# Kernel tuning notes

Measured on AMD Instinct MI355X. Metric: run time of the kernel, lower is better.

Reference implementation:

```python
import jax, jax.numpy as jnp
import numpy as np

D_MODEL = 64
SEQ_LEN = 9
MAX_SL = 50
TIMESTAMP = 56
ACTION_NUM = 300
BATCH = 65536


def setup_inputs() -> dict:
    key = jax.random.key(0)
    ks = jax.random.split(key, 8)
    input_actions = jax.random.randint(ks[0], (BATCH, SEQ_LEN), 0, ACTION_NUM + 1)
    emb_table = jax.random.normal(ks[1], (ACTION_NUM + 1, D_MODEL), jnp.float32) * 0.02
    emb_table = emb_table.at[0].set(0.0)  # padding_idx=0
    M_w = jax.random.normal(ks[2], (MAX_SL, D_MODEL, D_MODEL), jnp.float32) * 0.05
    M_b = jax.random.normal(ks[3], (MAX_SL, D_MODEL), jnp.float32) * 0.05
    W_w = jax.random.normal(ks[4], (TIMESTAMP, D_MODEL, D_MODEL), jnp.float32) * 0.05
    W_b = jax.random.normal(ks[5], (TIMESTAMP, D_MODEL), jnp.float32) * 0.05
    out_w = jax.random.normal(ks[6], (ACTION_NUM, D_MODEL), jnp.float32) * 0.05
    out_b = jax.random.normal(ks[7], (ACTION_NUM,), jnp.float32) * 0.05
    return {"input_actions": input_actions, "emb_table": emb_table,
            "M_w": M_w, "M_b": M_b, "W_w": W_w, "W_b": W_b,
            "out_w": out_w, "out_b": out_b}


def reference(input_actions, emb_table, M_w, M_b, W_w, W_b, out_w, out_b):
    B, S = input_actions.shape
    d = emb_table.shape[1]
    ae = emb_table[input_actions]              # [B, S, d]
    ae_t = jnp.transpose(ae, (1, 0, 2))        # [S, B, d]
    # per-timestep weight selection, matching M[min(i, len(M)-1)] and W[i % timeStamp]
    m_idx = jnp.minimum(jnp.arange(S), M_w.shape[0] - 1)
    w_idx = jnp.arange(S) % W_w.shape[0]
    Mw, Mb = M_w[m_idx], M_b[m_idx]            # [S, d, d], [S, d]
    Ww, Wb = W_w[w_idx], W_b[w_idx]

    def step(hl, xs):
        x, mw, mb, ww, wb = xs
        # torch Linear: y = x @ W.T + b
        hl = jax.nn.sigmoid(x @ mw.T + mb + hl @ ww.T + wb)
        return hl, None

    hl0 = jnp.zeros((B, d), ae.dtype)
    hl, _ = jax.lax.scan(step, hl0, (ae_t, Mw, Mb, Ww, Wb))
    return hl @ out_w.T + out_b               # [B, actionNum]
```

## Files before the change

### kernel.cpp

```cpp
#include <hip/hip_runtime.h>
#include <hip/hip_bf16.h>


#define SEQ     9
#define DMODEL  64
#define ANUM    300
#define RPB     128
#define LSTR    72

#define WS_MW   0
#define WS_OW   73728
#define WS_EMB  94208
#define WS_END  113472
#define WS_BSUM_BYTES (WS_END * 2)

typedef __attribute__((ext_vector_type(8))) short  bf16x8;
typedef __attribute__((ext_vector_type(4))) float  f32x4;

__device__ __forceinline__ unsigned short f2b(float f) {
    union { float f; unsigned int u; } x; x.f = f;
    unsigned int r = x.u + 0x7FFFu + ((x.u >> 16) & 1u);
    return (unsigned short)(r >> 16);
}

__device__ __forceinline__ float sigmoid_fast(float v) {
    return __builtin_amdgcn_rcpf(1.f + __expf(-v));
}

__device__ __forceinline__ void async16(const unsigned short* g, unsigned short* l) {
    __builtin_amdgcn_global_load_lds(
        (const __attribute__((address_space(1))) unsigned int*)g,
        (__attribute__((address_space(3))) unsigned int*)l, 16, 0, 0);
}

#define PP_TOTAL (73728 + 20480 + 19264 + 576)

__global__ void prepack(const float* __restrict__ Mw, const float* __restrict__ Ww,
                        const float* __restrict__ outw, const float* __restrict__ emb,
                        const float* __restrict__ Mb, const float* __restrict__ Wb,
                        unsigned short* __restrict__ wsb, float* __restrict__ bsum)
{
    int t = blockIdx.x * 256 + threadIdx.x;
    if (t < 73728) {
        int s    = t >> 13;
        int r    = t & 8191;
        int kind = r >> 12;
        int f    = r & 4095;
        int nt   = f >> 10;
        int kb   = (f >> 9) & 1;
        int lane = (f >> 3) & 63;
        int j    = f & 7;
        int nr   = nt * 16 + (lane & 15);
        int k    = kb * 32 + ((lane >> 4) << 3) + j;
        const float* src = kind ? Ww : Mw;
        wsb[WS_MW + t] = f2b(src[(s * DMODEL + nr) * DMODEL + k]);
        return;
    }
    t -= 73728;
    if (t < 20480) {
        int j    = t & 7;
        int lane = (t >> 3) & 63;
        int kb   = (t >> 9) & 1;
        int nt   = (t >> 10) & 3;
        int cc   = t >> 12;
        int col  = cc * 64 + nt * 16 + (lane & 15);
        int k    = kb * 32 + ((lane >> 4) << 3) + j;
        float v  = (col < ANUM) ? outw[col * DMODEL + k] : 0.f;
        wsb[WS_OW + t] = f2b(v);
        return;
    }
    t -= 20480;
    if (t < 19264) { wsb[WS_EMB + t] = f2b(emb[t]); return; }
    t -= 19264;
    if (t < 576)   { bsum[t] = Mb[t] + Wb[t]; }
}

__global__ __launch_bounds__(1024, 8)
void carnn_main(const int* __restrict__ acts,
                const unsigned short* __restrict__ wsb,
                const float* __restrict__ bsum,
                const float* __restrict__ outb,
                float* __restrict__ out)
{
    __shared__ unsigned short Wf[2][8192];
    __shared__ unsigned short Hl[2][RPB * LSTR];

    const int tid  = threadIdx.x;
    const int lane = tid & 63;
    const int wv   = tid >> 6;
    const int team = wv >> 1;
    const int half = wv & 1;
    const int lrow = lane & 15;
    const int quad = lane >> 4;

    const int brow = blockIdx.x * RPB + team * 16 + lrow;
    const int hoff = (team * 16 + lrow) * LSTR + quad * 8;

    for (int i = tid; i < RPB * LSTR; i += 1024) Hl[0][i] = 0;
    async16(wsb + WS_MW + tid * 8, &Wf[0][wv * 512]);

    const unsigned short* Eb = wsb + WS_EMB;
    int idcur = acts[brow * SEQ];

    __syncthreads();

    #pragma unroll
    for (int s = 0; s < SEQ; ++s) {
        const int rb = s & 1, wb = rb ^ 1;

        const bf16x8* ex = (const bf16x8*)(Eb + idcur * DMODEL);
        bf16x8 ax0 = ex[quad];
        bf16x8 ax1 = ex[4 + quad];

        if (s + 1 < SEQ) {
            idcur = acts[brow * SEQ + s + 1];
            async16(wsb + WS_MW + (s + 1) * 8192 + tid * 8, &Wf[wb][wv * 512]);
        } else {
            if (wv < 8) async16(wsb + WS_OW + tid * 8, &Wf[wb][wv * 512]);
        }

        bf16x8 ah0 = *(const bf16x8*)&Hl[rb][hoff];
        bf16x8 ah1 = *(const bf16x8*)&Hl[rb][hoff + 32];

        #pragma unroll
        for (int ntl = 0; ntl < 2; ++ntl) {
            const int nt = half * 2 + ntl;
            const unsigned short* Mf  = &Wf[rb][nt * 1024 + lane * 8];
            const unsigned short* Wfp = &Wf[rb][4096 + nt * 1024 + lane * 8];
            bf16x8 bm0 = *(const bf16x8*)Mf;
            bf16x8 bm1 = *(const bf16x8*)(Mf + 512);
            bf16x8 bw0 = *(const bf16x8*)Wfp;
            bf16x8 bw1 = *(const bf16x8*)(Wfp + 512);

            f32x4 acc = {0.f, 0.f, 0.f, 0.f};
            acc = __builtin_amdgcn_mfma_f32_16x16x32_bf16(ax0, bm0, acc, 0, 0, 0);
            acc = __builtin_amdgcn_mfma_f32_16x16x32_bf16(ax1, bm1, acc, 0, 0, 0);
            acc = __builtin_amdgcn_mfma_f32_16x16x32_bf16(ah0, bw0, acc, 0, 0, 0);
            acc = __builtin_amdgcn_mfma_f32_16x16x32_bf16(ah1, bw1, acc, 0, 0, 0);

            const int col  = nt * 16 + lrow;
            const float bias = bsum[s * DMODEL + col];
            const int wr = (team * 16 + quad * 4) * LSTR + col;
            #pragma unroll
            for (int r = 0; r < 4; ++r) {
                float h = sigmoid_fast(acc[r] + bias);
                Hl[wb][wr + r * LSTR] = f2b(h);
            }
        }
        __syncthreads();
    }

    bf16x8 ah0 = *(const bf16x8*)&Hl[1][hoff];
    bf16x8 ah1 = *(const bf16x8*)&Hl[1][hoff + 32];
    const int rowb = blockIdx.x * RPB + team * 16 + quad * 4;

    #pragma unroll
    for (int cc = 0; cc < 5; ++cc) {
        const int rbuf = (cc + 1) & 1;
        const int wbuf = rbuf ^ 1;
        if (cc + 1 < 5 && wv < 8)
            async16(wsb + WS_OW + (cc + 1) * 4096 + tid * 8, &Wf[wbuf][wv * 512]);

        #pragma unroll
        for (int ntl = 0; ntl < 2; ++ntl) {
            const int nt = half * 2 + ntl;
            const unsigned short* Of = &Wf[rbuf][nt * 1024 + lane * 8];
            bf16x8 b0 = *(const bf16x8*)Of;
            bf16x8 b1 = *(const bf16x8*)(Of + 512);
            f32x4 acc = {0.f, 0.f, 0.f, 0.f};
            acc = __builtin_amdgcn_mfma_f32_16x16x32_bf16(ah0, b0, acc, 0, 0, 0);
            acc = __builtin_amdgcn_mfma_f32_16x16x32_bf16(ah1, b1, acc, 0, 0, 0);

            const int col = cc * 64 + nt * 16 + lrow;
            if (col < ANUM) {
                const float bias = outb[col];
                #pragma unroll
                for (int r = 0; r < 4; ++r)
                    out[(rowb + r) * ANUM + col] = acc[r] + bias;
            }
        }
        if (cc + 1 < 5) __syncthreads();
    }
}

extern "C" void kernel_launch(void* const* d_in, const int* in_sizes, int n_in,
                              void* d_out, int out_size, void* d_ws, size_t ws_size,
                              hipStream_t stream) {
    const int*   acts = (const int*)  d_in[0];
    const float* emb  = (const float*)d_in[1];
    const float* Mw   = (const float*)d_in[2];
    const float* Mb   = (const float*)d_in[3];
    const float* Ww   = (const float*)d_in[4];
    const float* Wb   = (const float*)d_in[5];
    const float* outw = (const float*)d_in[6];
    const float* outb = (const float*)d_in[7];
    float* out = (float*)d_out;
    (void)in_sizes; (void)n_in; (void)ws_size; (void)out_size;

    unsigned short* wsb = (unsigned short*)d_ws;
    float* bsum = (float*)((char*)d_ws + WS_BSUM_BYTES);

    prepack<<<(PP_TOTAL + 255) / 256, 256, 0, stream>>>(Mw, Ww, outw, emb, Mb, Wb, wsb, bsum);
    carnn_main<<<65536 / RPB, 1024, 0, stream>>>(acts, wsb, bsum, outb, out);
}
```

Before: 124.9 us.

## Halve block threads, give each wave two row tiles, read out_w from global

Cuts the block from 1024 to 512 threads. Each wave now processes two 16-row tiles and reuses the same weight fragments for both, so B-operand LDS reads are amortized. Step 0 skips the recurrent MFMAs and the Hl zero-init, since the hidden state starts at zero. The output projection reads the prepacked out_w fragments straight from global or L2 instead of double-buffering them through LDS, which removes the per-chunk barriers. In exchange, registers per thread rise and each block has fewer waves to hide latency.

New measurement: 128.1 us. 1.03x slower.

```diff
diff --git a/kernel.cpp b/kernel.cpp
--- a/kernel.cpp
+++ b/kernel.cpp
@@ -75,111 +75,135 @@
     if (t < 576)   { bsum[t] = Mb[t] + Wb[t]; }
 }
 
-__global__ __launch_bounds__(1024, 8)
+__global__ __launch_bounds__(512, 4)
 void carnn_main(const int* __restrict__ acts,
                 const unsigned short* __restrict__ wsb,
                 const float* __restrict__ bsum,
                 const float* __restrict__ outb,
                 float* __restrict__ out)
 {
-    __shared__ unsigned short Wf[2][8192];
-    __shared__ unsigned short Hl[2][RPB * LSTR];
+    __shared__ __align__(16) unsigned short Wf[2][8192];
+    __shared__ __align__(16) unsigned short Hl[2][RPB * LSTR];
 
     const int tid  = threadIdx.x;
     const int lane = tid & 63;
     const int wv   = tid >> 6;
-    const int team = wv >> 1;
+    const int rg   = wv >> 1;
     const int half = wv & 1;
     const int lrow = lane & 15;
     const int quad = lane >> 4;
 
-    const int brow = blockIdx.x * RPB + team * 16 + lrow;
-    const int hoff = (team * 16 + lrow) * LSTR + quad * 8;
-
-    for (int i = tid; i < RPB * LSTR; i += 1024) Hl[0][i] = 0;
-    async16(wsb + WS_MW + tid * 8, &Wf[0][wv * 512]);
+    const int rb0   = rg * 32 + lrow;
+    const int rb1   = rb0 + 16;
+    const int brow0 = blockIdx.x * RPB + rb0;
+    const int brow1 = brow0 + 16;
+    const int hoff0 = rb0 * LSTR + quad * 8;
+    const int hoff1 = rb1 * LSTR + quad * 8;
+
+    async16(wsb + WS_MW + tid * 8,        &Wf[0][wv * 512]);
+    async16(wsb + WS_MW + 4096 + tid * 8, &Wf[0][4096 + wv * 512]);
 
     const unsigned short* Eb = wsb + WS_EMB;
-    int idcur = acts[brow * SEQ];
+    int id0 = acts[brow0 * SEQ];
+    int id1 = acts[brow1 * SEQ];
 
     __syncthreads();
 
     #pragma unroll
     for (int s = 0; s < SEQ; ++s) {
-        const int rb = s & 1, wb = rb ^ 1;
-
-        const bf16x8* ex = (const bf16x8*)(Eb + idcur * DMODEL);
-        bf16x8 ax0 = ex[quad];
-        bf16x8 ax1 = ex[4 + quad];
+        const int rbuf = s & 1, wbuf = rbuf ^ 1;
+
+        const bf16x8* e0 = (const bf16x8*)(Eb + id0 * DMODEL);
+        const bf16x8* e1 = (const bf16x8*)(Eb + id1 * DMODEL);
+        bf16x8 ax00 = e0[quad], ax01 = e0[4 + quad];
+        bf16x8 ax10 = e1[quad], ax11 = e1[4 + quad];
 
         if (s + 1 < SEQ) {
-            idcur = acts[brow * SEQ + s + 1];
-            async16(wsb + WS_MW + (s + 1) * 8192 + tid * 8, &Wf[wb][wv * 512]);
-        } else {
-            if (wv < 8) async16(wsb + WS_OW + tid * 8, &Wf[wb][wv * 512]);
-        }
-
-        bf16x8 ah0 = *(const bf16x8*)&Hl[rb][hoff];
-        bf16x8 ah1 = *(const bf16x8*)&Hl[rb][hoff + 32];
+            id0 = acts[brow0 * SEQ + s + 1];
+            id1 = acts[brow1 * SEQ + s + 1];
+            async16(wsb + WS_MW + (s + 1) * 8192 + tid * 8,        &Wf[wbuf][wv * 512]);
+            async16(wsb + WS_MW + (s + 1) * 8192 + 4096 + tid * 8, &Wf[wbuf][4096 + wv * 512]);
+        }
+
+        bf16x8 ah00, ah01, ah10, ah11;
+        if (s > 0) {
+            ah00 = *(const bf16x8*)&Hl[rbuf][hoff0];
+            ah01 = *(const bf16x8*)&Hl[rbuf][hoff0 + 32];
+            ah10 = *(const bf16x8*)&Hl[rbuf][hoff1];
+            ah11 = *(const bf16x8*)&Hl[rbuf][hoff1 + 32];
+        }
 
         #pragma unroll
         for (int ntl = 0; ntl < 2; ++ntl) {
             const int nt = half * 2 + ntl;
-            const unsigned short* Mf  = &Wf[rb][nt * 1024 + lane * 8];
-            const unsigned short* Wfp = &Wf[rb][4096 + nt * 1024 + lane * 8];
+            const unsigned short* Mf = &Wf[rbuf][nt * 1024 + lane * 8];
             bf16x8 bm0 = *(const bf16x8*)Mf;
             bf16x8 bm1 = *(const bf16x8*)(Mf + 512);
-            bf16x8 bw0 = *(const bf16x8*)Wfp;
-            bf16x8 bw1 = *(const bf16x8*)(Wfp + 512);
-
-            f32x4 acc = {0.f, 0.f, 0.f, 0.f};
-            acc = __builtin_amdgcn_mfma_f32_16x16x32_bf16(ax0, bm0, acc, 0, 0, 0);
-            acc = __builtin_amdgcn_mfma_f32_16x16x32_bf16(ax1, bm1, acc, 0, 0, 0);
-            acc = __builtin_amdgcn_mfma_f32_16x16x32_bf16(ah0, bw0, acc, 0, 0, 0);
-            acc = __builtin_amdgcn_mfma_f32_16x16x32_bf16(ah1, bw1, acc, 0, 0, 0);
-
-            const int col  = nt * 16 + lrow;
+
+            f32x4 a0 = {0.f, 0.f, 0.f, 0.f};
+            f32x4 a1 = {0.f, 0.f, 0.f, 0.f};
+            a0 = __builtin_amdgcn_mfma_f32_16x16x32_bf16(ax00, bm0, a0, 0, 0, 0);
+            a0 = __builtin_amdgcn_mfma_f32_16x16x32_bf16(ax01, bm1, a0, 0, 0, 0);
+            a1 = __builtin_amdgcn_mfma_f32_16x16x32_bf16(ax10, bm0, a1, 0, 0, 0);
+            a1 = __builtin_amdgcn_mfma_f32_16x16x32_bf16(ax11, bm1, a1, 0, 0, 0);
+            if (s > 0) {
+                const unsigned short* Wp = &Wf[rbuf][4096 + nt * 1024 + lane * 8];
+                bf16x8 bw0 = *(const bf16x8*)Wp;
+                bf16x8 bw1 = *(const bf16x8*)(Wp + 512);
+                a0 = __builtin_amdgcn_mfma_f32_16x16x32_bf16(ah00, bw0, a0, 0, 0, 0);
+                a0 = __builtin_amdgcn_mfma_f32_16x16x32_bf16(ah01, bw1, a0, 0, 0, 0);
+                a1 = __builtin_amdgcn_mfma_f32_16x16x32_bf16(ah10, bw0, a1, 0, 0, 0);
+                a1 = __builtin_amdgcn_mfma_f32_16x16x32_bf16(ah11, bw1, a1, 0, 0, 0);
+            }
+
+            const int col   = nt * 16 + lrow;
             const float bias = bsum[s * DMODEL + col];
-            const int wr = (team * 16 + quad * 4) * LSTR + col;
+            const int wr0 = (rg * 32 + quad * 4) * LSTR + col;
+            const int wr1 = wr0 + 16 * LSTR;
             #pragma unroll
             for (int r = 0; r < 4; ++r) {
-                float h = sigmoid_fast(acc[r] + bias);
-                Hl[wb][wr + r * LSTR] = f2b(h);
+                Hl[wbuf][wr0 + r * LSTR] = f2b(sigmoid_fast(a0[r] + bias));
+                Hl[wbuf][wr1 + r * LSTR] = f2b(sigmoid_fast(a1[r] + bias));
             }
         }
         __syncthreads();
     }
 
-    bf16x8 ah0 = *(const bf16x8*)&Hl[1][hoff];
-    bf16x8 ah1 = *(const bf16x8*)&Hl[1][hoff + 32];
-    const int rowb = blockIdx.x * RPB + team * 16 + quad * 4;
+    bf16x8 ah00 = *(const bf16x8*)&Hl[1][hoff0];
+    bf16x8 ah01 = *(const bf16x8*)&Hl[1][hoff0 + 32];
+    bf16x8 ah10 = *(const bf16x8*)&Hl[1][hoff1];
+    bf16x8 ah11 = *(const bf16x8*)&Hl[1][hoff1 + 32];
+
+    const unsigned short* OWg = wsb + WS_OW;
+    const int rowb0 = blockIdx.x * RPB + rg * 32 + quad * 4;
+    const int rowb1 = rowb0 + 16;
 
     #pragma unroll
     for (int cc = 0; cc < 5; ++cc) {
-        const int rbuf = (cc + 1) & 1;
-        const int wbuf = rbuf ^ 1;
-        if (cc + 1 < 5 && wv < 8)
-            async16(wsb + WS_OW + (cc + 1) * 4096 + tid * 8, &Wf[wbuf][wv * 512]);
-
         #pragma unroll
         for (int ntl = 0; ntl < 2; ++ntl) {
             const int nt = half * 2 + ntl;
-            const unsigned short* Of = &Wf[rbuf][nt * 1024 + lane * 8];
+            const unsigned short* Of = OWg + cc * 4096 + nt * 1024 + lane * 8;
             bf16x8 b0 = *(const bf16x8*)Of;
             bf16x8 b1 = *(const bf16x8*)(Of + 512);
-            f32x4 acc = {0.f, 0.f, 0.f, 0.f};
-            acc = __builtin_amdgcn_mfma_f32_16x16x32_bf16(ah0, b0, acc, 0, 0, 0);
-            acc = __builtin_amdgcn_mfma_f32_16x16x32_bf16(ah1, b1, acc, 0, 0, 0);
+
+            f32x4 a0 = {0.f, 0.f, 0.f, 0.f};
+            f32x4 a1 = {0.f, 0.f, 0.f, 0.f};
+            a0 = __builtin_amdgcn_mfma_f32_16x16x32_bf16(ah00, b0, a0, 0, 0, 0);
+            a0 = __builtin_amdgcn_mfma_f32_16x16x32_bf16(ah01, b1, a0, 0, 0, 0);
+            a1 = __builtin_amdgcn_mfma_f32_16x16x32_bf16(ah10, b0, a1, 0, 0, 0);
+            a1 = __builtin_amdgcn_mfma_f32_16x16x32_bf16(ah11, b1, a1, 0, 0, 0);
 
             const int col = cc * 64 + nt * 16 + lrow;
             if (col < ANUM) {
                 const float bias = outb[col];
                 #pragma unroll
-                for (int r = 0; r < 4; ++r)
-                    out[(rowb + r) * ANUM + col] = acc[r] + bias;
+                for (int r = 0; r < 4; ++r) {
+                    out[(rowb0 + r) * ANUM + col] = a0[r] + bias;
+                    out[(rowb1 + r) * ANUM + col] = a1[r] + bias;
+                }
             }
         }
-        if (cc + 1 < 5) __syncthreads();
     }
 }
 
@@ -201,5 +225,5 @@
     float* bsum = (float*)((char*)d_ws + WS_BSUM_BYTES);
 
     prepack<<<(PP_TOTAL + 255) / 256, 256, 0, stream>>>(Mw, Ww, outw, emb, Mb, Wb, wsb, bsum);
-    carnn_main<<<65536 / RPB, 1024, 0, stream>>>(acts, wsb, bsum, outb, out);
-}
+    carnn_main<<<65536 / RPB, 512, 0, stream>>>(acts, wsb, bsum, outb, out);
+}
```

## Preload all step weights to LDS, per-wave rows, drop per-step block barriers

Applied to the files above, without the earlier changes.

Each block now loads most of the recurrence weights and bias sums into LDS once at the start. Each wave owns 16 batch rows and computes all 64 hidden columns itself, so the per-step __syncthreads barriers disappear and the hidden state lives in a swizzled per-wave LDS slab. The MFMA operands are transposed so weights act as A and activations as B, which gives contiguous packed output writes and vector float4 stores in the output projection. The output projection now reads out_w straight from global or L2 instead of staging it in LDS. In exchange the block uses about 158KB of LDS, which limits occupancy to one block per CU, the last step's weights are read from global memory, and the block count halves to 256.

Measured after the change: 120.4 us. 3.6% less time.

```diff
diff --git a/kernel.cpp b/kernel.cpp
--- a/kernel.cpp
+++ b/kernel.cpp
@@ -5,8 +5,6 @@
 #define SEQ     9
 #define DMODEL  64
 #define ANUM    300
-#define RPB     128
-#define LSTR    72
 
 #define WS_MW   0
 #define WS_OW   73728
@@ -14,8 +12,14 @@
 #define WS_END  113472
 #define WS_BSUM_BYTES (WS_END * 2)
 
+#define BSOFF   61440
+#define HSOFF   62592
+#define SLTOT   78976
+
 typedef __attribute__((ext_vector_type(8))) short  bf16x8;
 typedef __attribute__((ext_vector_type(4))) float  f32x4;
+
+#define MFMA __builtin_amdgcn_mfma_f32_16x16x32_bf16
 
 __device__ __forceinline__ unsigned short f2b(float f) {
     union { float f; unsigned int u; } x; x.f = f;
@@ -75,111 +79,115 @@
     if (t < 576)   { bsum[t] = Mb[t] + Wb[t]; }
 }
 
-__global__ __launch_bounds__(1024, 8)
+__global__ __launch_bounds__(1024, 4)
 void carnn_main(const int* __restrict__ acts,
                 const unsigned short* __restrict__ wsb,
                 const float* __restrict__ bsum,
                 const float* __restrict__ outb,
                 float* __restrict__ out)
 {
-    __shared__ unsigned short Wf[2][8192];
-    __shared__ unsigned short Hl[2][RPB * LSTR];
+    __shared__ __align__(16) unsigned short SL[SLTOT];
 
     const int tid  = threadIdx.x;
     const int lane = tid & 63;
     const int wv   = tid >> 6;
-    const int team = wv >> 1;
-    const int half = wv & 1;
     const int lrow = lane & 15;
     const int quad = lane >> 4;
 
-    const int brow = blockIdx.x * RPB + team * 16 + lrow;
-    const int hoff = (team * 16 + lrow) * LSTR + quad * 8;
-
-    for (int i = tid; i < RPB * LSTR; i += 1024) Hl[0][i] = 0;
-    async16(wsb + WS_MW + tid * 8, &Wf[0][wv * 512]);
+    const int brow = (blockIdx.x * 16 + wv) * 16 + lrow;
+    const int rowS = brow * SEQ;
+
+    for (int c = wv; c < 120; c += 16) {
+        const int goff = (c < 8) ? (c * 512) : ((c + 8) * 512);
+        async16(wsb + WS_MW + goff + lane * 8, &SL[c * 512]);
+    }
+    {
+        const unsigned short* bs = (const unsigned short*)bsum;
+        if (wv == 13) async16(bs + lane * 8,         &SL[BSOFF]);
+        if (wv == 14) async16(bs + 512 + lane * 8,   &SL[BSOFF + 512]);
+        if (wv == 15 && lane < 16)
+                      async16(bs + 1024 + lane * 8,  &SL[BSOFF + 1024]);
+    }
 
     const unsigned short* Eb = wsb + WS_EMB;
-    int idcur = acts[brow * SEQ];
+    int idc = acts[rowS];
+    bf16x8 xc0 = *(const bf16x8*)(Eb + idc * DMODEL + quad * 8);
+    bf16x8 xc1 = *(const bf16x8*)(Eb + idc * DMODEL + 32 + quad * 8);
+    int idn = acts[rowS + 1];
+
+    char* const SB = (char*)SL;
+    const int swz    = (lrow & 7) << 4;
+    const int hbyte  = HSOFF * 2 + wv * 2048 + lrow * 128;
+    const int rbyte0 = hbyte + ((quad * 16) ^ swz);
+    const int rbyte1 = hbyte + ((64 + quad * 16) ^ swz);
 
     __syncthreads();
+
+    const float* BSf = (const float*)&SL[BSOFF];
 
     #pragma unroll
     for (int s = 0; s < SEQ; ++s) {
-        const int rb = s & 1, wb = rb ^ 1;
-
-        const bf16x8* ex = (const bf16x8*)(Eb + idcur * DMODEL);
-        bf16x8 ax0 = ex[quad];
-        bf16x8 ax1 = ex[4 + quad];
-
+        bf16x8 xn0, xn1;
         if (s + 1 < SEQ) {
-            idcur = acts[brow * SEQ + s + 1];
-            async16(wsb + WS_MW + (s + 1) * 8192 + tid * 8, &Wf[wb][wv * 512]);
-        } else {
-            if (wv < 8) async16(wsb + WS_OW + tid * 8, &Wf[wb][wv * 512]);
+            xn0 = *(const bf16x8*)(Eb + idn * DMODEL + quad * 8);
+            xn1 = *(const bf16x8*)(Eb + idn * DMODEL + 32 + quad * 8);
+            if (s + 2 < SEQ) idn = acts[rowS + s + 2];
         }
-
-        bf16x8 ah0 = *(const bf16x8*)&Hl[rb][hoff];
-        bf16x8 ah1 = *(const bf16x8*)&Hl[rb][hoff + 32];
+        bf16x8 h0, h1;
+        if (s > 0) {
+            h0 = *(const bf16x8*)(SB + rbyte0);
+            h1 = *(const bf16x8*)(SB + rbyte1);
+        }
+        const unsigned short* WB;
+        if (s == 0)     WB = &SL[0];
+        else if (s < 8) WB = &SL[4096 + (s - 1) * 8192];
+        else            WB = wsb + WS_MW + 8 * 8192;
 
         #pragma unroll
-        for (int ntl = 0; ntl < 2; ++ntl) {
-            const int nt = half * 2 + ntl;
-            const unsigned short* Mf  = &Wf[rb][nt * 1024 + lane * 8];
-            const unsigned short* Wfp = &Wf[rb][4096 + nt * 1024 + lane * 8];
-            bf16x8 bm0 = *(const bf16x8*)Mf;
-            bf16x8 bm1 = *(const bf16x8*)(Mf + 512);
-            bf16x8 bw0 = *(const bf16x8*)Wfp;
-            bf16x8 bw1 = *(const bf16x8*)(Wfp + 512);
-
-            f32x4 acc = {0.f, 0.f, 0.f, 0.f};
-            acc = __builtin_amdgcn_mfma_f32_16x16x32_bf16(ax0, bm0, acc, 0, 0, 0);
-            acc = __builtin_amdgcn_mfma_f32_16x16x32_bf16(ax1, bm1, acc, 0, 0, 0);
-            acc = __builtin_amdgcn_mfma_f32_16x16x32_bf16(ah0, bw0, acc, 0, 0, 0);
-            acc = __builtin_amdgcn_mfma_f32_16x16x32_bf16(ah1, bw1, acc, 0, 0, 0);
-
-            const int col  = nt * 16 + lrow;
-            const float bias = bsum[s * DMODEL + col];
-            const int wr = (team * 16 + quad * 4) * LSTR + col;
-            #pragma unroll
-            for (int r = 0; r < 4; ++r) {
-                float h = sigmoid_fast(acc[r] + bias);
-                Hl[wb][wr + r * LSTR] = f2b(h);
+        for (int nt = 0; nt < 4; ++nt) {
+            const unsigned short* Mf = WB + nt * 1024 + lane * 8;
+            bf16x8 am0 = *(const bf16x8*)Mf;
+            bf16x8 am1 = *(const bf16x8*)(Mf + 512);
+            f32x4 acc = *(const f32x4*)(BSf + s * 64 + nt * 16 + quad * 4);
+            acc = MFMA(am0, xc0, acc, 0, 0, 0);
+            acc = MFMA(am1, xc1, acc, 0, 0, 0);
+            if (s > 0) {
+                const unsigned short* Wf = WB + 4096 + nt * 1024 + lane * 8;
+                bf16x8 aw0 = *(const bf16x8*)Wf;
+                bf16x8 aw1 = *(const bf16x8*)(Wf + 512);
+                acc = MFMA(aw0, h0, acc, 0, 0, 0);
+                acc = MFMA(aw1, h1, acc, 0, 0, 0);
             }
+            unsigned int u0 = (unsigned int)f2b(sigmoid_fast(acc[0]))
+                            | ((unsigned int)f2b(sigmoid_fast(acc[1])) << 16);
+            unsigned int u1 = (unsigned int)f2b(sigmoid_fast(acc[2]))
+                            | ((unsigned int)f2b(sigmoid_fast(acc[3])) << 16);
+            *(uint2*)(SB + hbyte + ((nt * 32 + quad * 8) ^ swz)) = make_uint2(u0, u1);
         }
-        __syncthreads();
-    }
-
-    bf16x8 ah0 = *(const bf16x8*)&Hl[1][hoff];
-    bf16x8 ah1 = *(const bf16x8*)&Hl[1][hoff + 32];
-    const int rowb = blockIdx.x * RPB + team * 16 + quad * 4;
+        if (s + 1 < SEQ) { xc0 = xn0; xc1 = xn1; }
+    }
+
+    bf16x8 h0 = *(const bf16x8*)(SB + rbyte0);
+    bf16x8 h1 = *(const bf16x8*)(SB + rbyte1);
+    const unsigned short* OWg = wsb + WS_OW;
+    float* orow = out + brow * ANUM;
 
     #pragma unroll
-    for (int cc = 0; cc < 5; ++cc) {
-        const int rbuf = (cc + 1) & 1;
-        const int wbuf = rbuf ^ 1;
-        if (cc + 1 < 5 && wv < 8)
-            async16(wsb + WS_OW + (cc + 1) * 4096 + tid * 8, &Wf[wbuf][wv * 512]);
-
-        #pragma unroll
-        for (int ntl = 0; ntl < 2; ++ntl) {
-            const int nt = half * 2 + ntl;
-            const unsigned short* Of = &Wf[rbuf][nt * 1024 + lane * 8];
-            bf16x8 b0 = *(const bf16x8*)Of;
-            bf16x8 b1 = *(const bf16x8*)(Of + 512);
-            f32x4 acc = {0.f, 0.f, 0.f, 0.f};
-            acc = __builtin_amdgcn_mfma_f32_16x16x32_bf16(ah0, b0, acc, 0, 0, 0);
-            acc = __builtin_amdgcn_mfma_f32_16x16x32_bf16(ah1, b1, acc, 0, 0, 0);
-
-            const int col = cc * 64 + nt * 16 + lrow;
-            if (col < ANUM) {
-                const float bias = outb[col];
-                #pragma unroll
-                for (int r = 0; r < 4; ++r)
-                    out[(rowb + r) * ANUM + col] = acc[r] + bias;
-            }
-        }
-        if (cc + 1 < 5) __syncthreads();
+    for (int t = 0; t < 19; ++t) {
+        const int cc = t >> 2, nt = t & 3;
+        const unsigned short* Of = OWg + cc * 4096 + nt * 1024 + lane * 8;
+        bf16x8 a0 = *(const bf16x8*)Of;
+        bf16x8 a1 = *(const bf16x8*)(Of + 512);
+        const int col0 = cc * 64 + nt * 16 + quad * 4;
+
+        f32x4 acc;
+        if (col0 < ANUM) acc = *(const f32x4*)(outb + col0);
+        else             acc = (f32x4){0.f, 0.f, 0.f, 0.f};
+        acc = MFMA(a0, h0, acc, 0, 0, 0);
+        acc = MFMA(a1, h1, acc, 0, 0, 0);
+
+        if (col0 < ANUM)
+            *(f32x4*)(orow + col0) = acc;
     }
 }
 
@@ -201,5 +209,5 @@
     float* bsum = (float*)((char*)d_ws + WS_BSUM_BYTES);
 
     prepack<<<(PP_TOTAL + 255) / 256, 256, 0, stream>>>(Mw, Ww, outw, emb, Mb, Wb, wsb, bsum);
-    carnn_main<<<65536 / RPB, 1024, 0, stream>>>(acts, wsb, bsum, outb, out);
-}
+    carnn_main<<<65536 / 256, 1024, 0, stream>>>(acts, wsb, bsum, outb, out);
+}
```
